# Kernel tuning notes

Hardware: AMD Instinct MI355X
Metric: run time of the kernel (lower is better)

## Reference

```python
import jax, jax.numpy as jnp
import numpy as np

N_NODES = 50000
N_RAND_EDGES = 800000
LEAKY_SLOPE = 0.2


def gat_layer(x, edge_index, W, a_src, a_dst, b, num_heads):
    """Multi-head GAT layer. W: [Din, Dout]; heads split Dout; concat output."""
    N = x.shape[0]
    Dout = W.shape[1]
    Dh = Dout // num_heads
    z = (x @ W).reshape(N, num_heads, Dh)                      # [N,H,Dh]
    src = edge_index[0]
    dst = edge_index[1]
    alpha_src = jnp.einsum('nhd,hd->nh', z, a_src)             # [N,H]
    alpha_dst = jnp.einsum('nhd,hd->nh', z, a_dst)             # [N,H]
    e = jax.nn.leaky_relu(alpha_src[src] + alpha_dst[dst], LEAKY_SLOPE)  # [E,H]
    # segment softmax over incoming edges of each dst node
    m = jax.ops.segment_max(e, dst, num_segments=N)            # [N,H]
    e = jnp.exp(e - m[dst])
    denom = jax.ops.segment_sum(e, dst, num_segments=N)        # [N,H]
    alpha = e / (denom[dst] + 1e-16)                           # [E,H]
    msg = z[src] * alpha[:, :, None]                           # [E,H,Dh]
    out = jax.ops.segment_sum(msg, dst, num_segments=N)        # [N,H,Dh]
    return out.reshape(N, Dout) + b


def setup_inputs() -> dict:
    key = jax.random.key(0)
    ks = jax.random.split(key, 12)
    input_dim, hidden_dim, num_classes, num_heads = 128, 64, 16, 8
    x = jax.random.normal(ks[0], (N_NODES, input_dim), dtype=jnp.float32)
    rand_edges = jax.random.randint(ks[1], (2, N_RAND_EDGES), 0, N_NODES, dtype=jnp.int32)
    self_loops = jnp.tile(jnp.arange(N_NODES, dtype=jnp.int32), (2, 1))
    edge_indices = jnp.concatenate([rand_edges, self_loops], axis=1)   # [2, 850000]

    def glorot(k, shape):
        fan = sum(shape[-2:]) if len(shape) > 1 else shape[0]
        return jax.random.normal(k, shape, dtype=jnp.float32) * (2.0 / fan) ** 0.5

    W1 = glorot(ks[2], (input_dim, hidden_dim))
    a_src1 = glorot(ks[3], (num_heads, hidden_dim // num_heads))
    a_dst1 = glorot(ks[4], (num_heads, hidden_dim // num_heads))
    b1 = jnp.zeros((hidden_dim,), dtype=jnp.float32)
    W2 = glorot(ks[5], (hidden_dim, num_classes))
    a_src2 = glorot(ks[6], (1, num_classes))
    a_dst2 = glorot(ks[7], (1, num_classes))
    b2 = jnp.zeros((num_classes,), dtype=jnp.float32)
    return {"x": x, "edge_indices": edge_indices,
            "W1": W1, "a_src1": a_src1, "a_dst1": a_dst1, "b1": b1,
            "W2": W2, "a_src2": a_src2, "a_dst2": a_dst2, "b2": b2}


def reference(x, edge_indices, W1, a_src1, a_dst1, b1, W2, a_src2, a_dst2, b2):
    # Dropout is identity in eval mode.
    h = gat_layer(x, edge_indices, W1, a_src1, a_dst1, b1, num_heads=8)
    h = jax.nn.elu(h)
    return gat_layer(h, edge_indices, W2, a_src2, a_dst2, b2, num_heads=1)
```

## Files before the change

### kernel.cpp

```cpp
#include <hip/hip_runtime.h>
#include <hip/hip_fp16.h>


#define LRELU(v) ((v) > 0.f ? (v) : 0.2f * (v))

__global__ void kA(const float* __restrict__ x, const float* __restrict__ W1,
                   const float* __restrict__ a_src1, const float* __restrict__ a_dst1,
                   const int* __restrict__ src, const int* __restrict__ dst,
                   int* __restrict__ deg, int* __restrict__ csr,
                   __half* __restrict__ z1h, float* __restrict__ as1,
                   float* __restrict__ ad1, int N, int E) {
    __shared__ float xs[64][132];
    __shared__ float wt[64][132];
    __shared__ float avs[128];
    int b = blockIdx.x;
    int tid = threadIdx.x;
    bool is_gemm = (b < 1564) && ((b & 1) == 0);

    if (!is_gemm) {
        int rank = (b < 1564) ? (b >> 1) : (b - 782);
        for (int e = rank * 256 + tid; e < E; e += 1024 * 256) {
            int d = dst[e];
            int pos = atomicAdd(&deg[d], 1);
            if (pos < 64) csr[(d << 6) + pos] = src[e];
        }
        return;
    }

    int n0 = (b >> 1) * 64;
    for (int idx = tid; idx < 8192; idx += 256) {
        int k = idx >> 6, c = idx & 63;
        wt[c][k] = W1[idx];
    }
    for (int idx = tid; idx < 2048; idx += 256) {
        int r = idx >> 5, q = idx & 31;
        int n = n0 + r; if (n >= N) n = N - 1;
        float4 v = ((const float4*)(x + (size_t)n * 128))[q];
        *(float4*)&xs[r][q * 4] = v;
    }
    if (tid < 128) avs[tid] = (tid < 64) ? a_src1[tid] : a_dst1[tid - 64];
    __syncthreads();

    int rg = tid >> 4, cg2 = tid & 15;
    float acc[4][4] = {};
    for (int k4 = 0; k4 < 32; ++k4) {
        float4 xv[4], wv[4];
#pragma unroll
        for (int i = 0; i < 4; ++i) xv[i] = *(const float4*)&xs[rg * 4 + i][k4 * 4];
#pragma unroll
        for (int j = 0; j < 4; ++j) wv[j] = *(const float4*)&wt[cg2 * 4 + j][k4 * 4];
#pragma unroll
        for (int i = 0; i < 4; ++i)
#pragma unroll
            for (int j = 0; j < 4; ++j) {
                acc[i][j] += xv[i].x * wv[j].x;
                acc[i][j] += xv[i].y * wv[j].y;
                acc[i][j] += xv[i].z * wv[j].z;
                acc[i][j] += xv[i].w * wv[j].w;
            }
    }
    int h = cg2 >> 1, db = (cg2 & 1) * 4;
    float pas[4], pad_[4];
#pragma unroll
    for (int i = 0; i < 4; ++i) {
        float s = 0.f, dd = 0.f;
#pragma unroll
        for (int j = 0; j < 4; ++j) {
            s  += acc[i][j] * avs[h * 8 + db + j];
            dd += acc[i][j] * avs[64 + h * 8 + db + j];
        }
        pas[i] = s; pad_[i] = dd;
    }
#pragma unroll
    for (int i = 0; i < 4; ++i) {
        pas[i]  += __shfl_xor(pas[i], 1, 64);
        pad_[i] += __shfl_xor(pad_[i], 1, 64);
    }
#pragma unroll
    for (int i = 0; i < 4; ++i) {
        int n = n0 + rg * 4 + i;
        if (n < N) {
            union { __half2 h2[2]; uint2 u; } pk;
            pk.h2[0] = __floats2half2_rn(acc[i][0], acc[i][1]);
            pk.h2[1] = __floats2half2_rn(acc[i][2], acc[i][3]);
            *(uint2*)&z1h[(size_t)n * 64 + cg2 * 4] = pk.u;
            if ((cg2 & 1) == 0) {
                as1[(size_t)n * 8 + h] = pas[i];
                ad1[(size_t)n * 8 + h] = pad_[i];
            }
        }
    }
}

__global__ void kg1(const int* __restrict__ deg, const int* __restrict__ csr,
                    const float* __restrict__ as1, const float* __restrict__ ad1,
                    const __half* __restrict__ z1h, const float* __restrict__ b1,
                    const float* __restrict__ W2, const float* __restrict__ a_src2,
                    const float* __restrict__ a_dst2,
                    float* __restrict__ z2, float* __restrict__ as2,
                    float* __restrict__ ad2, int N) {
    __shared__ int s_idx[4][64];
    __shared__ float hs[4][64];
    int lane = threadIdx.x & 63, wid = threadIdx.x >> 6;
    int d = blockIdx.x * 4 + wid;
    if (d >= N) return;
    int q = lane & 7, g = lane >> 3;
    int cnt = min(deg[d], 64);
    float adv = ad1[(size_t)d * 8 + q];
    if (lane < cnt) s_idx[wid][lane] = csr[(d << 6) + lane];
    float a0 = 0.f, a1 = 0.f, a2 = 0.f, a3 = 0.f;
    float a4 = 0.f, a5 = 0.f, a6 = 0.f, a7 = 0.f, dsum = 0.f;
#pragma unroll 2
    for (int j = g; j < cnt; j += 8) {
        int s = s_idx[wid][j];
        float ev = as1[(size_t)s * 8 + q] + adv;
        float w = __expf(LRELU(ev));
        float4 raw = *(const float4*)(z1h + (size_t)s * 64 + q * 8);
        const __half2* hp = (const __half2*)&raw;
        float2 f0 = __half22float2(hp[0]), f1 = __half22float2(hp[1]);
        float2 f2 = __half22float2(hp[2]), f3 = __half22float2(hp[3]);
        a0 += w * f0.x; a1 += w * f0.y; a2 += w * f1.x; a3 += w * f1.y;
        a4 += w * f2.x; a5 += w * f2.y; a6 += w * f3.x; a7 += w * f3.y;
        dsum += w;
    }
#pragma unroll
    for (int m = 8; m <= 32; m <<= 1) {
        a0 += __shfl_xor(a0, m, 64); a1 += __shfl_xor(a1, m, 64);
        a2 += __shfl_xor(a2, m, 64); a3 += __shfl_xor(a3, m, 64);
        a4 += __shfl_xor(a4, m, 64); a5 += __shfl_xor(a5, m, 64);
        a6 += __shfl_xor(a6, m, 64); a7 += __shfl_xor(a7, m, 64);
        dsum += __shfl_xor(dsum, m, 64);
    }
    float inv = 1.f / dsum;
    float hv[8] = {a0 * inv + b1[q * 8 + 0], a1 * inv + b1[q * 8 + 1],
                   a2 * inv + b1[q * 8 + 2], a3 * inv + b1[q * 8 + 3],
                   a4 * inv + b1[q * 8 + 4], a5 * inv + b1[q * 8 + 5],
                   a6 * inv + b1[q * 8 + 6], a7 * inv + b1[q * 8 + 7]};
#pragma unroll
    for (int i = 0; i < 8; ++i) hv[i] = hv[i] > 0.f ? hv[i] : expm1f(hv[i]);
    if (g == 0) {
        *(float4*)&hs[wid][q * 8]     = make_float4(hv[0], hv[1], hv[2], hv[3]);
        *(float4*)&hs[wid][q * 8 + 4] = make_float4(hv[4], hv[5], hv[6], hv[7]);
    }
    int kq = lane >> 4, c = lane & 15;
    float zc = 0.f;
#pragma unroll
    for (int k = 0; k < 16; ++k)
        zc += hs[wid][kq * 16 + k] * W2[(kq * 16 + k) * 16 + c];
    zc += __shfl_xor(zc, 16, 64);
    zc += __shfl_xor(zc, 32, 64);
    float ps = zc * a_src2[c];
    float pd = zc * a_dst2[c];
#pragma unroll
    for (int m = 1; m < 16; m <<= 1) {
        ps += __shfl_xor(ps, m, 64);
        pd += __shfl_xor(pd, m, 64);
    }
    if (lane < 16) z2[(size_t)d * 16 + lane] = zc;
    if (lane == 0) { as2[d] = ps; ad2[d] = pd; }
}

__global__ void kg2(const int* __restrict__ deg, const int* __restrict__ csr,
                    const float* __restrict__ as2, const float* __restrict__ ad2,
                    const float* __restrict__ z2, const float* __restrict__ b2,
                    float* __restrict__ out, int N) {
    __shared__ int s_idx[4][64];
    int lane = threadIdx.x & 63, wid = threadIdx.x >> 6;
    int d = blockIdx.x * 4 + wid;
    if (d >= N) return;
    int q = lane & 3, g = lane >> 2;
    int cnt = min(deg[d], 64);
    float adv = ad2[d];
    if (lane < cnt) s_idx[wid][lane] = csr[(d << 6) + lane];
    float ax = 0.f, ay = 0.f, az = 0.f, aw = 0.f, dsum = 0.f;
#pragma unroll 2
    for (int j = g; j < cnt; j += 16) {
        int s = s_idx[wid][j];
        float ev = as2[s] + adv;
        float w = __expf(LRELU(ev));
        float4 zv = *(const float4*)(z2 + (size_t)s * 16 + q * 4);
        ax += w * zv.x; ay += w * zv.y; az += w * zv.z; aw += w * zv.w;
        dsum += w;
    }
#pragma unroll
    for (int m = 4; m <= 32; m <<= 1) {
        ax += __shfl_xor(ax, m, 64); ay += __shfl_xor(ay, m, 64);
        az += __shfl_xor(az, m, 64); aw += __shfl_xor(aw, m, 64);
        dsum += __shfl_xor(dsum, m, 64);
    }
    if (g == 0) {
        float inv = 1.f / dsum;
        float4 o = make_float4(ax * inv + b2[q * 4], ay * inv + b2[q * 4 + 1],
                               az * inv + b2[q * 4 + 2], aw * inv + b2[q * 4 + 3]);
        *(float4*)&out[(size_t)d * 16 + q * 4] = o;
    }
}

extern "C" void kernel_launch(void* const* d_in, const int* in_sizes, int n_in,
                              void* d_out, int out_size, void* d_ws, size_t ws_size,
                              hipStream_t stream) {
    const float* x      = (const float*)d_in[0];
    const int*   ei     = (const int*)d_in[1];
    const float* W1     = (const float*)d_in[2];
    const float* a_src1 = (const float*)d_in[3];
    const float* a_dst1 = (const float*)d_in[4];
    const float* b1     = (const float*)d_in[5];
    const float* W2     = (const float*)d_in[6];
    const float* a_src2 = (const float*)d_in[7];
    const float* a_dst2 = (const float*)d_in[8];
    const float* b2     = (const float*)d_in[9];
    float* out = (float*)d_out;

    const int N = in_sizes[0] / 128;
    const int E = in_sizes[1] / 2;
    const int* src = ei;
    const int* dst = ei + E;

    float* ws = (float*)d_ws;
    size_t off = 0;
    __half* z1h = (__half*)(ws + off); off += (size_t)N * 32;
    float* as1 = ws + off; off += (size_t)N * 8;
    float* ad1 = ws + off; off += (size_t)N * 8;
    float* z2  = ws + off; off += (size_t)N * 16;
    float* as2 = ws + off; off += (size_t)N;
    float* ad2 = ws + off; off += (size_t)N;
    int* csr = (int*)(ws + off); off += (size_t)N * 64;
    int* deg = (int*)(ws + off); off += (size_t)N;

    hipMemsetAsync(deg, 0, (size_t)N * sizeof(int), stream);

    kA<<<1806, 256, 0, stream>>>(x, W1, a_src1, a_dst1, src, dst, deg, csr,
                                 z1h, as1, ad1, N, E);
    kg1<<<(N + 3) / 4, 256, 0, stream>>>(deg, csr, as1, ad1, z1h, b1, W2,
                                         a_src2, a_dst2, z2, as2, ad2, N);
    kg2<<<(N + 3) / 4, 256, 0, stream>>>(deg, csr, as2, ad2, z2, b2, out, N);
}
```

Measured before the change: 185.9 us.

## Build CSR via two-pass bucketed partition instead of global atomics

Replaces the per-edge global atomicAdd scatter into a padded CSR with a two-phase build. Partition blocks in kA histogram edges into 196 destination buckets of 256 nodes using shared-memory atomics, reserve space per bucket with one global atomic, and write packed (src,dstlow) pairs. A new kernel kB then builds each bucket's CSR with shared atomics and writes deg directly. This removes contended global atomics and the deg memset, but adds an extra kernel launch and pass over the edges, and fixed bucket capacity (5120) risks dropping edges on skewed inputs.

```diff
diff --git a/kernel.cpp b/kernel.cpp
--- a/kernel.cpp
+++ b/kernel.cpp
@@ -3,11 +3,14 @@
 
 
 #define LRELU(v) ((v) > 0.f ? (v) : 0.2f * (v))
+
+#define NB   196
+#define BCAP 5120
 
 __global__ void kA(const float* __restrict__ x, const float* __restrict__ W1,
                    const float* __restrict__ a_src1, const float* __restrict__ a_dst1,
                    const int* __restrict__ src, const int* __restrict__ dst,
-                   int* __restrict__ deg, int* __restrict__ csr,
+                   int* __restrict__ bcnt, int* __restrict__ pairs,
                    __half* __restrict__ z1h, float* __restrict__ as1,
                    float* __restrict__ ad1, int N, int E) {
     __shared__ float xs[64][132];
@@ -15,19 +18,39 @@
     __shared__ float avs[128];
     int b = blockIdx.x;
     int tid = threadIdx.x;
-    bool is_gemm = (b < 1564) && ((b & 1) == 0);
-
-    if (!is_gemm) {
-        int rank = (b < 1564) ? (b >> 1) : (b - 782);
-        for (int e = rank * 256 + tid; e < E; e += 1024 * 256) {
-            int d = dst[e];
-            int pos = atomicAdd(&deg[d], 1);
-            if (pos < 64) csr[(d << 6) + pos] = src[e];
+    bool is_part = ((b % 5) == 4);
+
+    if (is_part) {
+        int* hist  = (int*)&xs[0][0];
+        int* base_ = hist + 256;
+        int* cur   = hist + 512;
+        int rank = b / 5;
+        if (tid < NB) hist[tid] = 0;
+        __syncthreads();
+        int chunk = (E + NB - 1) / NB;
+        int e0 = rank * chunk;
+        int e1 = min(e0 + chunk, E);
+        for (int e = e0 + tid; e < e1; e += 256)
+            atomicAdd(&hist[dst[e] >> 8], 1);
+        __syncthreads();
+        if (tid < NB) {
+            base_[tid] = atomicAdd(&bcnt[tid], hist[tid]);
+            cur[tid] = 0;
+        }
+        __syncthreads();
+        for (int e = e0 + tid; e < e1; e += 256) {
+            int d = dst[e], s = src[e];
+            int bk = d >> 8;
+            int r = atomicAdd(&cur[bk], 1);
+            int idx = base_[bk] + r;
+            if (idx < BCAP) pairs[bk * BCAP + idx] = (s << 8) | (d & 255);
         }
         return;
     }
 
-    int n0 = (b >> 1) * 64;
+    int tile = (b / 5) * 4 + (b % 5);
+    if (tile >= 782) return;
+    int n0 = tile * 64;
     for (int idx = tid; idx < 8192; idx += 256) {
         int k = idx >> 6, c = idx & 63;
         wt[c][k] = W1[idx];
@@ -90,6 +113,26 @@
             }
         }
     }
+}
+
+__global__ void kB(const int* __restrict__ bcnt, const int* __restrict__ pairs,
+                   int* __restrict__ deg, int* __restrict__ csr, int N) {
+    __shared__ int cur[256];
+    int b = blockIdx.x;
+    int tid = threadIdx.x;
+    cur[tid] = 0;
+    __syncthreads();
+    int nb = min(bcnt[b], BCAP);
+    const int* p = pairs + b * BCAP;
+    for (int i = tid; i < nb; i += 256) {
+        int v = p[i];
+        int off = v & 255, s = v >> 8;
+        int r = atomicAdd(&cur[off], 1);
+        if (r < 64) csr[(((b << 8) + off) << 6) + r] = s;
+    }
+    __syncthreads();
+    int d = (b << 8) + tid;
+    if (d < N) deg[d] = cur[tid];
 }
 
 __global__ void kg1(const int* __restrict__ deg, const int* __restrict__ csr,
@@ -226,11 +269,14 @@
     float* ad2 = ws + off; off += (size_t)N;
     int* csr = (int*)(ws + off); off += (size_t)N * 64;
     int* deg = (int*)(ws + off); off += (size_t)N;
-
-    hipMemsetAsync(deg, 0, (size_t)N * sizeof(int), stream);
-
-    kA<<<1806, 256, 0, stream>>>(x, W1, a_src1, a_dst1, src, dst, deg, csr,
-                                 z1h, as1, ad1, N, E);
+    int* pairs = (int*)(ws + off); off += (size_t)NB * BCAP;
+    int* bcnt = (int*)(ws + off); off += NB;
+
+    hipMemsetAsync(bcnt, 0, (size_t)NB * sizeof(int), stream);
+
+    kA<<<980, 256, 0, stream>>>(x, W1, a_src1, a_dst1, src, dst, bcnt, pairs,
+                                z1h, as1, ad1, N, E);
+    kB<<<NB, 256, 0, stream>>>(bcnt, pairs, deg, csr, N);
     kg1<<<(N + 3) / 4, 256, 0, stream>>>(deg, csr, as1, ad1, z1h, b1, W2,
                                          a_src2, a_dst2, z2, as2, ad2, N);
     kg2<<<(N + 3) / 4, 256, 0, stream>>>(deg, csr, as2, ad2, z2, b2, out, N);
```

After: 179.7 us. 1.03x faster.
